# Kernel optimization log

Hardware: AMD Instinct MI355X
Metric: run time of the kernel (lower is better)

## Reference

```python
import jax, jax.numpy as jnp
import numpy as np

H_KV = 8          # num_key_value_heads (hard-coded in module)
N_HEADS = 32
HEAD_DIM = 128
GROUPS = N_HEADS // H_KV
EPS = 1e-05
ROPE_THETA = 10000.0


def rotate_half(x):
    x1, x2 = jnp.split(x, 2, axis=-1)
    return jnp.concatenate((-x2, x1), axis=-1)


def rms_norm(x, w, eps=EPS):
    xf = x.astype(jnp.float32)
    var = jnp.mean(xf * xf, axis=-1, keepdims=True)
    return (w * (xf * jax.lax.rsqrt(var + eps))).astype(x.dtype)


def setup_inputs() -> dict:
    key = jax.random.key(0)
    k1, k2, k3 = jax.random.split(key, 3)
    B, S, D = 2, 2048, 4096
    hidden_states = jax.random.normal(k1, (B, S, D), dtype=jnp.float32)
    # RoPE tables (what custom_pos_emb carries)
    inv_freq = 1.0 / (ROPE_THETA ** (jnp.arange(0, HEAD_DIM, 2, dtype=jnp.float32) / HEAD_DIM))
    t = jnp.arange(S, dtype=jnp.float32)
    freqs = jnp.outer(t, inv_freq)                 # [S, HEAD_DIM/2]
    emb = jnp.concatenate((freqs, freqs), axis=-1)  # [S, HEAD_DIM]
    cos = jnp.cos(emb)[None]                        # [1, S, HEAD_DIM]
    sin = jnp.sin(emb)[None]
    w_qkv = jax.random.normal(k2, (6144, D), dtype=jnp.float32) * 0.02
    w_o = jax.random.normal(k3, (D, D), dtype=jnp.float32) * 0.02
    q_norm_w = jnp.ones((HEAD_DIM,), dtype=jnp.float32)
    k_norm_w = jnp.ones((HEAD_DIM,), dtype=jnp.float32)
    return {"hidden_states": hidden_states, "cos": cos, "sin": sin,
            "w_qkv": w_qkv, "w_o": w_o, "q_norm_w": q_norm_w, "k_norm_w": k_norm_w}


def reference(hidden_states, cos, sin, w_qkv, w_o, q_norm_w, k_norm_w):
    B, S, D = hidden_states.shape
    qkv = hidden_states @ w_qkv.T                                    # [B,S,6144]
    qkv = qkv.reshape(B, S, H_KV, GROUPS + 2, HEAD_DIM)
    q = qkv[:, :, :, :GROUPS]                                        # [B,S,Hkv,G,d]
    k = qkv[:, :, :, GROUPS]                                         # [B,S,Hkv,d]
    v = qkv[:, :, :, GROUPS + 1]                                     # [B,S,Hkv,d]
    # to [B, heads, S, d]
    q = q.reshape(B, S, N_HEADS, HEAD_DIM).transpose(0, 2, 1, 3)     # [B,Hq,S,d]
    k = k.transpose(0, 2, 1, 3)                                      # [B,Hkv,S,d]
    v = v.transpose(0, 2, 1, 3)
    # RoPE (cos/sin: [1,S,d] -> unsqueeze head dim)
    c = cos[:, None]  # [1,1,S,d]
    s = sin[:, None]
    q = q * c + rotate_half(q) * s
    k = k * c + rotate_half(k) * s
    # per-head RMSNorm
    q = rms_norm(q, q_norm_w)
    k = rms_norm(k, k_norm_w)
    # GQA attention without materializing repeated K/V
    qg = q.reshape(B, H_KV, GROUPS, S, HEAD_DIM)
    scale = 1.0 / np.sqrt(HEAD_DIM).astype(np.float32)
    scores = jnp.einsum('bkgqd,bksd->bkgqs', qg, k) * scale          # [B,Hkv,G,S,S]
    probs = jax.nn.softmax(scores, axis=-1)
    out = jnp.einsum('bkgqs,bksd->bkgqd', probs, v)                  # [B,Hkv,G,S,d]
    out = out.reshape(B, N_HEADS, S, HEAD_DIM).transpose(0, 2, 1, 3).reshape(B, S, D)
    return out @ w_o.T
```

## Files before the change

kernel.cpp:

```cpp
#include <hip/hip_runtime.h>
#include <hip/hip_bf16.h>

typedef __attribute__((ext_vector_type(8))) short short8;
typedef __attribute__((ext_vector_type(4))) short short4v;
typedef __attribute__((ext_vector_type(4))) float floatx4;
typedef __attribute__((ext_vector_type(4))) unsigned int uintx4;

static __device__ __forceinline__ short bf16bits(float f) {
    __hip_bfloat16 h = __float2bfloat16(f);
    return __builtin_bit_cast(short, h);
}

static __device__ __forceinline__ unsigned int cvtpk(float lo, float hi) {
    unsigned int r;
    asm("v_cvt_pk_bf16_f32 %0, %1, %2" : "=v"(r) : "v"(lo), "v"(hi));
    return r;
}

#define GLDS(g, l) __builtin_amdgcn_global_load_lds( \
    (const __attribute__((address_space(1))) void*)(g), \
    (__attribute__((address_space(3))) void*)(l), 16, 0, 0)

__global__ __launch_bounds__(256) void cvt_bf16(
    const float* __restrict__ src, __hip_bfloat16* __restrict__ dst)
{
    size_t i = ((size_t)blockIdx.x * 256 + threadIdx.x) * 8;
    floatx4 f0 = *(const floatx4*)(src + i);
    floatx4 f1 = *(const floatx4*)(src + i + 4);
    short8 s;
#pragma unroll
    for (int j = 0; j < 4; j++) { s[j] = bf16bits(f0[j]); s[j + 4] = bf16bits(f1[j]); }
    *(short8*)((short*)dst + i) = s;
}

template<typename CT>
__global__ __launch_bounds__(256) void gemm_bt_fast(
    const __hip_bfloat16* __restrict__ A,
    const __hip_bfloat16* __restrict__ W,
    CT* __restrict__ C, int M, int N, int K)
{
    __shared__ alignas(16) short lA[128 * 64];
    __shared__ alignas(16) short lB[128 * 64];

    const int tid  = threadIdx.x;
    const int wave = tid >> 6;
    const int lane = tid & 63;
    const int quad = lane >> 4;
    const int l16  = lane & 15;

    const int m0 = blockIdx.x * 128;
    const int n0 = blockIdx.y * 128;
    const int wm = (wave & 1) * 64;
    const int wn = (wave >> 1) * 64;

    const int srow = lane >> 3;
    const int sblk = (lane & 7) ^ srow;
    const int scol = sblk * 8;

    const short* Ag = (const short*)A;
    const short* Wg = (const short*)W;

    floatx4 acc[4][4];
#pragma unroll
    for (int i = 0; i < 4; i++)
#pragma unroll
        for (int j = 0; j < 4; j++) acc[i][j] = (floatx4)0.0f;

    for (int k0 = 0; k0 < K; k0 += 64) {
        __syncthreads();
#pragma unroll
        for (int i = 0; i < 4; i++) {
            int c   = wave * 4 + i;
            int row = c * 8 + srow;
            GLDS(Ag + (size_t)(m0 + row) * K + k0 + scol, &lA[c * 512]);
            GLDS(Wg + (size_t)(n0 + row) * K + k0 + scol, &lB[c * 512]);
        }
        __syncthreads();
#pragma unroll
        for (int kk2 = 0; kk2 < 2; kk2++) {
            const int pb = ((kk2 * 4 + quad) ^ (l16 & 7)) * 8;
            short8 af[4], bf[4];
#pragma unroll
            for (int i = 0; i < 4; i++)
                af[i] = *(const short8*)(&lA[(wm + i * 16 + l16) * 64 + pb]);
#pragma unroll
            for (int j = 0; j < 4; j++)
                bf[j] = *(const short8*)(&lB[(wn + j * 16 + l16) * 64 + pb]);
#pragma unroll
            for (int i = 0; i < 4; i++)
#pragma unroll
                for (int j = 0; j < 4; j++)
                    acc[i][j] = __builtin_amdgcn_mfma_f32_16x16x32_bf16(
                        af[i], bf[j], acc[i][j], 0, 0, 0);
        }
    }
#pragma unroll
    for (int i = 0; i < 4; i++)
#pragma unroll
        for (int j = 0; j < 4; j++) {
            int gm = m0 + wm + i * 16 + quad * 4;
            int gn = n0 + wn + j * 16 + l16;
#pragma unroll
            for (int r = 0; r < 4; r++) {
                float v = acc[i][j][r];
                if constexpr (sizeof(CT) == 2)
                    C[(size_t)(gm + r) * N + gn] = (CT)__float2bfloat16(v);
                else
                    C[(size_t)(gm + r) * N + gn] = (CT)v;
            }
        }
}

template<bool AF32, typename CT>
__global__ __launch_bounds__(256) void gemm_bt_slow(
    const void* __restrict__ A,
    const float* __restrict__ Wf,
    CT* __restrict__ C, int M, int N, int K)
{
    __shared__ alignas(16) short lA[128 * 72];
    __shared__ alignas(16) short lB[128 * 72];

    const int tid  = threadIdx.x;
    const int wave = tid >> 6;
    const int lane = tid & 63;
    const int quad = lane >> 4;
    const int l16  = lane & 15;

    const int m0 = blockIdx.x * 128;
    const int n0 = blockIdx.y * 128;
    const int wm = (wave & 1) * 64;
    const int wn = (wave >> 1) * 64;

    floatx4 acc[4][4];
#pragma unroll
    for (int i = 0; i < 4; i++)
#pragma unroll
        for (int j = 0; j < 4; j++) acc[i][j] = (floatx4)0.0f;

    const short* Ab = (const short*)A;
    const float* Af = (const float*)A;

    for (int k0 = 0; k0 < K; k0 += 64) {
        __syncthreads();
#pragma unroll
        for (int i = 0; i < 4; i++) {
            int chunk = tid + i * 256;
            int row = chunk >> 3;
            int cc  = chunk & 7;
            if (AF32) {
                const float* src = Af + (size_t)(m0 + row) * K + k0 + cc * 8;
                floatx4 f0 = *(const floatx4*)(src);
                floatx4 f1 = *(const floatx4*)(src + 4);
                short8 s;
#pragma unroll
                for (int j = 0; j < 4; j++) { s[j] = bf16bits(f0[j]); s[j + 4] = bf16bits(f1[j]); }
                *(short8*)(&lA[row * 72 + cc * 8]) = s;
            } else {
                *(short8*)(&lA[row * 72 + cc * 8]) =
                    *(const short8*)(Ab + (size_t)(m0 + row) * K + k0 + cc * 8);
            }
            const float* src = Wf + (size_t)(n0 + row) * K + k0 + cc * 8;
            floatx4 f0 = *(const floatx4*)(src);
            floatx4 f1 = *(const floatx4*)(src + 4);
            short8 s;
#pragma unroll
            for (int j = 0; j < 4; j++) { s[j] = bf16bits(f0[j]); s[j + 4] = bf16bits(f1[j]); }
            *(short8*)(&lB[row * 72 + cc * 8]) = s;
        }
        __syncthreads();
#pragma unroll
        for (int kk = 0; kk < 64; kk += 32) {
            short8 af[4], bf[4];
#pragma unroll
            for (int i = 0; i < 4; i++)
                af[i] = *(const short8*)(&lA[(wm + i * 16 + l16) * 72 + kk + quad * 8]);
#pragma unroll
            for (int j = 0; j < 4; j++)
                bf[j] = *(const short8*)(&lB[(wn + j * 16 + l16) * 72 + kk + quad * 8]);
#pragma unroll
            for (int i = 0; i < 4; i++)
#pragma unroll
                for (int j = 0; j < 4; j++)
                    acc[i][j] = __builtin_amdgcn_mfma_f32_16x16x32_bf16(
                        af[i], bf[j], acc[i][j], 0, 0, 0);
        }
    }
#pragma unroll
    for (int i = 0; i < 4; i++)
#pragma unroll
        for (int j = 0; j < 4; j++) {
            int gm = m0 + wm + i * 16 + quad * 4;
            int gn = n0 + wn + j * 16 + l16;
#pragma unroll
            for (int r = 0; r < 4; r++) {
                float v = acc[i][j][r];
                if constexpr (sizeof(CT) == 2)
                    C[(size_t)(gm + r) * N + gn] = (CT)__float2bfloat16(v);
                else
                    C[(size_t)(gm + r) * N + gn] = (CT)v;
            }
        }
}

__global__ __launch_bounds__(256) void rope_norm(
    __hip_bfloat16* __restrict__ qkv,
    const float* __restrict__ cosb,
    const float* __restrict__ sinb,
    const float* __restrict__ qw,
    const float* __restrict__ kw)
{
    int wid  = blockIdx.x * 4 + (threadIdx.x >> 6);
    int lane = threadIdx.x & 63;
    int token = wid / 40;
    int idx   = wid % 40;
    int s = token & 2047;

    int off;
    const float* w;
    if (idx < 32) { off = (idx >> 2) * 768 + (idx & 3) * 128; w = qw; }
    else          { off = (idx - 32) * 768 + 512;             w = kw; }

    short* p = (short*)(qkv + (size_t)token * 6144 + off);
    int d = lane * 2;

    unsigned int pv = *(const unsigned int*)(p + d);
    float x0 = __builtin_bit_cast(float, pv << 16);
    float x1 = __builtin_bit_cast(float, pv & 0xffff0000u);

    float ox0 = __shfl_xor(x0, 32, 64);
    float ox1 = __shfl_xor(x1, 32, 64);

    float2 cv = *(const float2*)(cosb + s * 128 + d);
    float2 sv = *(const float2*)(sinb + s * 128 + d);
    float sgn = (lane < 32) ? -1.0f : 1.0f;
    float y0 = fmaf(sgn * ox0, sv.x, x0 * cv.x);
    float y1 = fmaf(sgn * ox1, sv.y, x1 * cv.y);

    float ss = y0 * y0 + y1 * y1;
#pragma unroll
    for (int m = 1; m < 64; m <<= 1) ss += __shfl_xor(ss, m, 64);
    float r = rsqrtf(ss * (1.0f / 128.0f) + 1e-5f);

    float2 wv = *(const float2*)(w + d);
    unsigned int out = (unsigned int)(unsigned short)bf16bits(y0 * r * wv.x)
                     | ((unsigned int)(unsigned short)bf16bits(y1 * r * wv.y) << 16);
    *(unsigned int*)(p + d) = out;
}

__global__ __launch_bounds__(256) void vtrans(
    const __hip_bfloat16* __restrict__ qkv, __hip_bfloat16* __restrict__ Vt)
{
    __shared__ alignas(16) short lT[64 * 136];

    const int bid   = blockIdx.x;
    const int stile = bid & 31;
    const int kvh   = (bid >> 5) & 7;
    const int b     = bid >> 8;
    const int tid   = threadIdx.x;
    const size_t voff = (size_t)kvh * 768 + 640;
    const short* qkvs = (const short*)qkv;

#pragma unroll
    for (int i = 0; i < 4; i++) {
        int chunk = tid + i * 256;
        int t  = chunk >> 4;
        int dc = chunk & 15;
        size_t tok = (size_t)(b * 2048 + stile * 64 + t);
        *(short8*)(&lT[t * 136 + dc * 8]) =
            *(const short8*)(qkvs + tok * 6144 + voff + dc * 8);
    }
    __syncthreads();

    int d  = tid >> 1;
    int kh = (tid & 1) * 32;
    short* out = (short*)Vt + ((size_t)((b * 8 + kvh) * 128 + d)) * 2048
               + stile * 64 + kh;
#pragma unroll
    for (int jb = 0; jb < 4; jb++) {
        short8 s;
#pragma unroll
        for (int j = 0; j < 8; j++) s[j] = lT[(kh + jb * 8 + j) * 136 + d];
        *(short8*)(out + jb * 8) = s;
    }
}

__global__ __launch_bounds__(256, 2) void attn_kernel(
    const __hip_bfloat16* __restrict__ qkv,
    const __hip_bfloat16* __restrict__ Vt,
    __hip_bfloat16* __restrict__ attn_out)
{
    __shared__ alignas(16) short lK[2][64 * 128];
    __shared__ alignas(16) short lVt[2][128 * 64];

    const int bid0 = blockIdx.x;
    const int bid  = (bid0 & 7) * 128 + (bid0 >> 3);
    const int qt   = bid & 15;
    const int h    = (bid >> 4) & 31;
    const int b    = bid >> 9;
    const int kvh  = h >> 2;
    const int lane = threadIdx.x & 63;
    const int wave = threadIdx.x >> 6;
    const int quad = lane >> 4;
    const int l16  = lane & 15;

    const size_t qoff = (size_t)kvh * 768 + (size_t)(h & 3) * 128;
    const size_t koff = (size_t)kvh * 768 + 512;
    const short* qkvs = (const short*)qkv;
    const short* Vts  = (const short*)Vt + ((size_t)(b * 8 + kvh) * 128) * 2048;

    short8 qf[2][4];
#pragma unroll
    for (int t = 0; t < 2; t++) {
        const int qrow = qt * 128 + wave * 32 + t * 16 + l16;
        const size_t qtok = (size_t)(b * 2048 + qrow);
#pragma unroll
        for (int kk = 0; kk < 4; kk++)
            qf[t][kk] = *(const short8*)(qkvs + qtok * 6144 + qoff + kk * 32 + quad * 8);
    }

    floatx4 o[2][8];
#pragma unroll
    for (int t = 0; t < 2; t++)
#pragma unroll
        for (int n = 0; n < 8; n++) o[t][n] = (floatx4)0.0f;
    float mrow[2] = { -3.0e4f, -3.0e4f };
    float lsum[2] = { 0.0f, 0.0f };

    const float scale2 = 0.08838834764831845f * 1.4426950408889634f;
    const float THR2   = 11.5418f;

    const int k_row = lane >> 4;
    const int v_row = lane >> 3;
    const int v_blk = (lane & 7) ^ v_row;

    const int srcA = l16 + ((lane & 16) << 1);
    const int srcB = srcA + 16;
    const bool hi2 = (quad >> 1) != 0;

#pragma unroll
    for (int i = 0; i < 4; i++) {
        int c = wave * 4 + i;
        int k_blk = (lane & 15) ^ ((c * 4 + k_row) & 15);
        size_t tok = (size_t)(b * 2048 + c * 4 + k_row);
        GLDS(qkvs + tok * 6144 + koff + k_blk * 8, &lK[0][c * 512]);
        int d = c * 8 + v_row;
        GLDS(Vts + (size_t)d * 2048 + v_blk * 8, &lVt[0][c * 512]);
    }

    int cur = 0;
    for (int kt = 0; kt < 32; kt++) {
        __syncthreads();

        if (kt < 31) {
            short* nK = &lK[cur ^ 1][0];
            short* nV = &lVt[cur ^ 1][0];
#pragma unroll
            for (int i = 0; i < 4; i++) {
                int c = wave * 4 + i;
                int k_blk = (lane & 15) ^ ((c * 4 + k_row) & 15);
                size_t tok = (size_t)(b * 2048 + (kt + 1) * 64 + c * 4 + k_row);
                GLDS(qkvs + tok * 6144 + koff + k_blk * 8, nK + c * 512);
                int d = c * 8 + v_row;
                GLDS(Vts + (size_t)d * 2048 + (kt + 1) * 64 + v_blk * 8, nV + c * 512);
            }
        }

        const short* lKc = &lK[cur][0];
        const short* lVc = &lVt[cur][0];

        floatx4 sc[2][4];
#pragma unroll
        for (int t = 0; t < 2; t++)
#pragma unroll
            for (int n = 0; n < 4; n++) sc[t][n] = (floatx4)0.0f;
#pragma unroll
        for (int kk = 0; kk < 4; kk++) {
#pragma unroll
            for (int n = 0; n < 4; n++) {
                short8 kf = *(const short8*)(
                    &lKc[(n * 16 + l16) * 128 + (((kk * 4 + quad) ^ l16)) * 8]);
                sc[0][n] = __builtin_amdgcn_mfma_f32_16x16x32_bf16(kf, qf[0][kk], sc[0][n], 0, 0, 0);
                sc[1][n] = __builtin_amdgcn_mfma_f32_16x16x32_bf16(kf, qf[1][kk], sc[1][n], 0, 0, 0);
            }
        }

        short8 pb[2][2];
#pragma unroll
        for (int t = 0; t < 2; t++) {
            float ma = fmaxf(fmaxf(sc[t][0][0], sc[t][0][1]), fmaxf(sc[t][0][2], sc[t][0][3]));
            float mb = fmaxf(fmaxf(sc[t][1][0], sc[t][1][1]), fmaxf(sc[t][1][2], sc[t][1][3]));
            float mc = fmaxf(fmaxf(sc[t][2][0], sc[t][2][1]), fmaxf(sc[t][2][2], sc[t][2][3]));
            float md = fmaxf(fmaxf(sc[t][3][0], sc[t][3][1]), fmaxf(sc[t][3][2], sc[t][3][3]));
            float mr = fmaxf(fmaxf(ma, mb), fmaxf(mc, md));
            mr = fmaxf(mr, __shfl_xor(mr, 16, 64));
            mr = fmaxf(mr, __shfl_xor(mr, 32, 64));
            float mx = mr * scale2;

            int grown = mx > mrow[t] + THR2;
            if (__any(grown)) {
                float mn = fmaxf(mrow[t], mx);
                float alpha = exp2f(mrow[t] - mn);
                mrow[t] = mn;
                lsum[t] *= alpha;
#pragma unroll
                for (int n = 0; n < 8; n++)
#pragma unroll
                    for (int r = 0; r < 4; r++) o[t][n][r] *= alpha;
            }

            const float nm = -mrow[t];
            float ps = 0.0f;
            unsigned int pk[4][2];
#pragma unroll
            for (int n = 0; n < 4; n++) {
#pragma unroll
                for (int r = 0; r < 4; r++) {
                    float pv = exp2f(fmaf(sc[t][n][r], scale2, nm));
                    sc[t][n][r] = pv;
                    ps += pv;
                }
                pk[n][0] = cvtpk(sc[t][n][0], sc[t][n][1]);
                pk[n][1] = cvtpk(sc[t][n][2], sc[t][n][3]);
            }
            lsum[t] += ps;

#pragma unroll
            for (int kk2 = 0; kk2 < 2; kk2++) {
                unsigned int a0 = __shfl(pk[2 * kk2][0],     srcA, 64);
                unsigned int a1 = __shfl(pk[2 * kk2 + 1][0], srcA, 64);
                unsigned int a2 = __shfl(pk[2 * kk2][1],     srcA, 64);
                unsigned int a3 = __shfl(pk[2 * kk2 + 1][1], srcA, 64);
                unsigned int c0 = __shfl(pk[2 * kk2][0],     srcB, 64);
                unsigned int c1 = __shfl(pk[2 * kk2 + 1][0], srcB, 64);
                unsigned int c2 = __shfl(pk[2 * kk2][1],     srcB, 64);
                unsigned int c3 = __shfl(pk[2 * kk2 + 1][1], srcB, 64);
                uintx4 u;
                u[0] = hi2 ? a1 : a0;
                u[1] = hi2 ? a3 : a2;
                u[2] = hi2 ? c1 : c0;
                u[3] = hi2 ? c3 : c2;
                pb[t][kk2] = __builtin_bit_cast(short8, u);
            }
        }

#pragma unroll
        for (int kk2 = 0; kk2 < 2; kk2++) {
            const int pbv = ((kk2 * 4 + quad) ^ (l16 & 7)) * 8;
#pragma unroll
            for (int n = 0; n < 8; n++) {
                short8 vf = *(const short8*)(&lVc[(n * 16 + l16) * 64 + pbv]);
                o[0][n] = __builtin_amdgcn_mfma_f32_16x16x32_bf16(vf, pb[0][kk2], o[0][n], 0, 0, 0);
                o[1][n] = __builtin_amdgcn_mfma_f32_16x16x32_bf16(vf, pb[1][kk2], o[1][n], 0, 0, 0);
            }
        }

        cur ^= 1;
    }

    float inv[2];
#pragma unroll
    for (int t = 0; t < 2; t++) {
        float s = lsum[t];
        s += __shfl_xor(s, 16, 64);
        s += __shfl_xor(s, 32, 64);
        inv[t] = 1.0f / s;
    }

#pragma unroll
    for (int t = 0; t < 2; t++) {
        const int row = qt * 128 + wave * 32 + t * 16 + l16;
        const size_t tok = (size_t)(b * 2048 + row);
        short* outp = (short*)attn_out + tok * 4096 + h * 128 + quad * 4;
#pragma unroll
        for (int n = 0; n < 8; n++) {
            short4v s4;
#pragma unroll
            for (int r = 0; r < 4; r++) s4[r] = bf16bits(o[t][n][r] * inv[t]);
            *(short4v*)(outp + n * 16) = s4;
        }
    }
}

extern "C" void kernel_launch(void* const* d_in, const int* in_sizes, int n_in,
                              void* d_out, int out_size, void* d_ws, size_t ws_size,
                              hipStream_t stream) {
    const float* hidden = (const float*)d_in[0];
    const float* cosb   = (const float*)d_in[1];
    const float* sinb   = (const float*)d_in[2];
    const float* w_qkv  = (const float*)d_in[3];
    const float* w_o    = (const float*)d_in[4];
    const float* qw     = (const float*)d_in[5];
    const float* kw     = (const float*)d_in[6];

    char* ws = (char*)d_ws;
    __hip_bfloat16* qkv    = (__hip_bfloat16*)ws;
    __hip_bfloat16* attn_o = (__hip_bfloat16*)(ws + 50331648);
    __hip_bfloat16* hb  = (__hip_bfloat16*)(ws + 83886080);
    __hip_bfloat16* wb1 = (__hip_bfloat16*)(ws + 117440512);
    __hip_bfloat16* wb2 = (__hip_bfloat16*)(ws + 167772160);
    const size_t WS_FAST = 201326592;

    __hip_bfloat16* Vt = (__hip_bfloat16*)d_out;
    float* outp        = (float*)d_out;

    const bool fast = (ws_size >= WS_FAST);

    if (fast) {
        cvt_bf16<<<16777216 / 8 / 256, 256, 0, stream>>>(hidden, hb);
        cvt_bf16<<<25165824 / 8 / 256, 256, 0, stream>>>(w_qkv, wb1);
        cvt_bf16<<<16777216 / 8 / 256, 256, 0, stream>>>(w_o, wb2);
        dim3 g1(32, 48);
        gemm_bt_fast<__hip_bfloat16><<<g1, 256, 0, stream>>>(hb, wb1, qkv, 4096, 6144, 4096);
    } else {
        dim3 g1(32, 48);
        gemm_bt_slow<true, __hip_bfloat16><<<g1, 256, 0, stream>>>(hidden, w_qkv, qkv, 4096, 6144, 4096);
    }

    rope_norm<<<40960, 256, 0, stream>>>(qkv, cosb, sinb, qw, kw);

    vtrans<<<512, 256, 0, stream>>>(qkv, Vt);

    attn_kernel<<<1024, 256, 0, stream>>>(qkv, Vt, attn_o);

    dim3 g2(32, 32);
    if (fast) {
        gemm_bt_fast<float><<<g2, 256, 0, stream>>>(attn_o, wb2, outp, 4096, 4096, 4096);
    } else {
        gemm_bt_slow<false, float><<<g2, 256, 0, stream>>>(attn_o, w_o, outp, 4096, 4096, 4096);
    }
}
```

Baseline: 875.7 us.

## Replace bf16 GEMM with 256x256 double-buffered, phase-interleaved MFMA kernel

After: 925.1 us. +5.6%, slower.

```diff
diff --git a/kernel.cpp b/kernel.cpp
--- a/kernel.cpp
+++ b/kernel.cpp
@@ -34,13 +34,13 @@
 }
 
 template<typename CT>
-__global__ __launch_bounds__(256) void gemm_bt_fast(
+__global__ __launch_bounds__(512, 2) void gemm_bt_8ph(
     const __hip_bfloat16* __restrict__ A,
     const __hip_bfloat16* __restrict__ W,
     CT* __restrict__ C, int M, int N, int K)
 {
-    __shared__ alignas(16) short lA[128 * 64];
-    __shared__ alignas(16) short lB[128 * 64];
+    __shared__ alignas(16) short lA[2][256 * 64];
+    __shared__ alignas(16) short lB[2][256 * 64];
 
     const int tid  = threadIdx.x;
     const int wave = tid >> 6;
@@ -48,10 +48,10 @@
     const int quad = lane >> 4;
     const int l16  = lane & 15;
 
-    const int m0 = blockIdx.x * 128;
-    const int n0 = blockIdx.y * 128;
-    const int wm = (wave & 1) * 64;
-    const int wn = (wave >> 1) * 64;
+    const int m0 = blockIdx.x * 256;
+    const int n0 = blockIdx.y * 256;
+    const int wm = (wave >> 2) * 128;
+    const int wn = (wave & 3) * 64;
 
     const int srow = lane >> 3;
     const int sblk = (lane & 7) ^ srow;
@@ -60,42 +60,87 @@
     const short* Ag = (const short*)A;
     const short* Wg = (const short*)W;
 
-    floatx4 acc[4][4];
-#pragma unroll
-    for (int i = 0; i < 4; i++)
+    floatx4 acc[8][4];
+#pragma unroll
+    for (int i = 0; i < 8; i++)
 #pragma unroll
         for (int j = 0; j < 4; j++) acc[i][j] = (floatx4)0.0f;
 
-    for (int k0 = 0; k0 < K; k0 += 64) {
-        __syncthreads();
-#pragma unroll
-        for (int i = 0; i < 4; i++) {
-            int c   = wave * 4 + i;
-            int row = c * 8 + srow;
-            GLDS(Ag + (size_t)(m0 + row) * K + k0 + scol, &lA[c * 512]);
-            GLDS(Wg + (size_t)(n0 + row) * K + k0 + scol, &lB[c * 512]);
-        }
-        __syncthreads();
-#pragma unroll
-        for (int kk2 = 0; kk2 < 2; kk2++) {
-            const int pb = ((kk2 * 4 + quad) ^ (l16 & 7)) * 8;
+    const int NT = K >> 6;
+
+    auto stage = [&](int t1, int p, int dst) {
+        int c   = wave * 4 + p;
+        int row = c * 8 + srow;
+        int k0  = t1 << 6;
+        GLDS(Ag + (size_t)(m0 + row) * K + k0 + scol, &lA[dst][c * 512]);
+        GLDS(Wg + (size_t)(n0 + row) * K + k0 + scol, &lB[dst][c * 512]);
+    };
+
+#pragma unroll
+    for (int p = 0; p < 4; p++) stage(0, p, 0);
+
+    int cur = 0;
+    for (int t = 0; t < NT; t++) {
+        const bool more = (t + 1 < NT);
+
+        if (more) {
+            stage(t + 1, 0, cur ^ 1);
+            asm volatile("s_waitcnt vmcnt(2)" ::: "memory");
+        } else {
+            asm volatile("s_waitcnt vmcnt(0)" ::: "memory");
+        }
+        __builtin_amdgcn_s_barrier();
+        {
+            const int pb = ((0 * 4 + quad) ^ (l16 & 7)) * 8;
             short8 af[4], bf[4];
 #pragma unroll
-            for (int i = 0; i < 4; i++)
-                af[i] = *(const short8*)(&lA[(wm + i * 16 + l16) * 64 + pb]);
+            for (int ii = 0; ii < 4; ii++)
+                af[ii] = *(const short8*)(&lA[cur][(wm + ii * 16 + l16) * 64 + pb]);
 #pragma unroll
             for (int j = 0; j < 4; j++)
-                bf[j] = *(const short8*)(&lB[(wn + j * 16 + l16) * 64 + pb]);
-#pragma unroll
-            for (int i = 0; i < 4; i++)
+                bf[j] = *(const short8*)(&lB[cur][(wn + j * 16 + l16) * 64 + pb]);
+            __builtin_amdgcn_s_setprio(1);
+#pragma unroll
+            for (int ii = 0; ii < 4; ii++)
 #pragma unroll
                 for (int j = 0; j < 4; j++)
-                    acc[i][j] = __builtin_amdgcn_mfma_f32_16x16x32_bf16(
-                        af[i], bf[j], acc[i][j], 0, 0, 0);
-        }
-    }
-#pragma unroll
-    for (int i = 0; i < 4; i++)
+                    acc[ii][j] = __builtin_amdgcn_mfma_f32_16x16x32_bf16(
+                        af[ii], bf[j], acc[ii][j], 0, 0, 0);
+            __builtin_amdgcn_s_setprio(0);
+        }
+        __builtin_amdgcn_s_barrier();
+
+#pragma unroll
+        for (int p = 1; p < 4; p++) {
+            const int kk = p >> 1;
+            const int mh = p & 1;
+            const int pb = ((kk * 4 + quad) ^ (l16 & 7)) * 8;
+            short8 af[4], bf[4];
+#pragma unroll
+            for (int ii = 0; ii < 4; ii++)
+                af[ii] = *(const short8*)(
+                    &lA[cur][(wm + (mh * 4 + ii) * 16 + l16) * 64 + pb]);
+#pragma unroll
+            for (int j = 0; j < 4; j++)
+                bf[j] = *(const short8*)(&lB[cur][(wn + j * 16 + l16) * 64 + pb]);
+            if (more) stage(t + 1, p, cur ^ 1);
+            __builtin_amdgcn_s_barrier();
+            __builtin_amdgcn_s_setprio(1);
+#pragma unroll
+            for (int ii = 0; ii < 4; ii++)
+#pragma unroll
+                for (int j = 0; j < 4; j++)
+                    acc[mh * 4 + ii][j] = __builtin_amdgcn_mfma_f32_16x16x32_bf16(
+                        af[ii], bf[j], acc[mh * 4 + ii][j], 0, 0, 0);
+            __builtin_amdgcn_s_setprio(0);
+            __builtin_amdgcn_s_barrier();
+        }
+
+        cur ^= 1;
+    }
+
+#pragma unroll
+    for (int i = 0; i < 8; i++)
 #pragma unroll
         for (int j = 0; j < 4; j++) {
             int gm = m0 + wm + i * 16 + quad * 4;
@@ -509,8 +554,8 @@
         cvt_bf16<<<16777216 / 8 / 256, 256, 0, stream>>>(hidden, hb);
         cvt_bf16<<<25165824 / 8 / 256, 256, 0, stream>>>(w_qkv, wb1);
         cvt_bf16<<<16777216 / 8 / 256, 256, 0, stream>>>(w_o, wb2);
-        dim3 g1(32, 48);
-        gemm_bt_fast<__hip_bfloat16><<<g1, 256, 0, stream>>>(hb, wb1, qkv, 4096, 6144, 4096);
+        dim3 g1(16, 24);
+        gemm_bt_8ph<__hip_bfloat16><<<g1, 512, 0, stream>>>(hb, wb1, qkv, 4096, 6144, 4096);
     } else {
         dim3 g1(32, 48);
         gemm_bt_slow<true, __hip_bfloat16><<<g1, 256, 0, stream>>>(hidden, w_qkv, qkv, 4096, 6144, 4096);
@@ -522,10 +567,11 @@
 
     attn_kernel<<<1024, 256, 0, stream>>>(qkv, Vt, attn_o);
 
-    dim3 g2(32, 32);
     if (fast) {
-        gemm_bt_fast<float><<<g2, 256, 0, stream>>>(attn_o, wb2, outp, 4096, 4096, 4096);
+        dim3 g2(16, 16);
+        gemm_bt_8ph<float><<<g2, 512, 0, stream>>>(attn_o, wb2, outp, 4096, 4096, 4096);
     } else {
+        dim3 g2(32, 32);
         gemm_bt_slow<false, float><<<g2, 256, 0, stream>>>(attn_o, w_o, outp, 4096, 4096, 4096);
     }
 }
```

## Add double-buffered 256x256-tile GEMM for output projection

Applied to the files above, without the earlier changes.

Result: faster. 837.1 us (-4.4%).

```diff
diff --git a/kernel.cpp b/kernel.cpp
--- a/kernel.cpp
+++ b/kernel.cpp
@@ -96,6 +96,98 @@
     }
 #pragma unroll
     for (int i = 0; i < 4; i++)
+#pragma unroll
+        for (int j = 0; j < 4; j++) {
+            int gm = m0 + wm + i * 16 + quad * 4;
+            int gn = n0 + wn + j * 16 + l16;
+#pragma unroll
+            for (int r = 0; r < 4; r++) {
+                float v = acc[i][j][r];
+                if constexpr (sizeof(CT) == 2)
+                    C[(size_t)(gm + r) * N + gn] = (CT)__float2bfloat16(v);
+                else
+                    C[(size_t)(gm + r) * N + gn] = (CT)v;
+            }
+        }
+}
+
+template<typename CT>
+__global__ __launch_bounds__(512, 2) void gemm_bt_dbuf(
+    const __hip_bfloat16* __restrict__ A,
+    const __hip_bfloat16* __restrict__ W,
+    CT* __restrict__ C, int M, int N, int K)
+{
+    __shared__ alignas(16) short lA[2][256 * 64];
+    __shared__ alignas(16) short lB[2][256 * 64];
+
+    const int tid  = threadIdx.x;
+    const int wave = tid >> 6;
+    const int lane = tid & 63;
+    const int quad = lane >> 4;
+    const int l16  = lane & 15;
+
+    const int m0 = blockIdx.x * 256;
+    const int n0 = blockIdx.y * 256;
+    const int wm = (wave >> 2) * 128;
+    const int wn = (wave & 3) * 64;
+
+    const int srow = lane >> 3;
+    const int sblk = (lane & 7) ^ srow;
+    const int scol = sblk * 8;
+
+    const short* Ag = (const short*)A;
+    const short* Wg = (const short*)W;
+
+    floatx4 acc[8][4];
+#pragma unroll
+    for (int i = 0; i < 8; i++)
+#pragma unroll
+        for (int j = 0; j < 4; j++) acc[i][j] = (floatx4)0.0f;
+
+    const int NT = K >> 6;
+
+    auto stage = [&](int t1, int dst) {
+        int k0 = t1 << 6;
+#pragma unroll
+        for (int p = 0; p < 4; p++) {
+            int c   = wave * 4 + p;
+            int row = c * 8 + srow;
+            GLDS(Ag + (size_t)(m0 + row) * K + k0 + scol, &lA[dst][c * 512]);
+            GLDS(Wg + (size_t)(n0 + row) * K + k0 + scol, &lB[dst][c * 512]);
+        }
+    };
+
+    stage(0, 0);
+
+    int cur = 0;
+    for (int t = 0; t < NT; t++) {
+        __syncthreads();
+        if (t + 1 < NT) stage(t + 1, cur ^ 1);
+
+#pragma unroll
+        for (int kk = 0; kk < 2; kk++) {
+            const int pb = ((kk * 4 + quad) ^ (l16 & 7)) * 8;
+            short8 bf[4], af[8];
+#pragma unroll
+            for (int j = 0; j < 4; j++)
+                bf[j] = *(const short8*)(&lB[cur][(wn + j * 16 + l16) * 64 + pb]);
+#pragma unroll
+            for (int i = 0; i < 8; i++)
+                af[i] = *(const short8*)(&lA[cur][(wm + i * 16 + l16) * 64 + pb]);
+            __builtin_amdgcn_s_setprio(1);
+#pragma unroll
+            for (int i = 0; i < 8; i++)
+#pragma unroll
+                for (int j = 0; j < 4; j++)
+                    acc[i][j] = __builtin_amdgcn_mfma_f32_16x16x32_bf16(
+                        af[i], bf[j], acc[i][j], 0, 0, 0);
+            __builtin_amdgcn_s_setprio(0);
+        }
+        cur ^= 1;
+    }
+
+#pragma unroll
+    for (int i = 0; i < 8; i++)
 #pragma unroll
         for (int j = 0; j < 4; j++) {
             int gm = m0 + wm + i * 16 + quad * 4;
@@ -522,10 +614,11 @@
 
     attn_kernel<<<1024, 256, 0, stream>>>(qkv, Vt, attn_o);
 
-    dim3 g2(32, 32);
     if (fast) {
-        gemm_bt_fast<float><<<g2, 256, 0, stream>>>(attn_o, wb2, outp, 4096, 4096, 4096);
+        dim3 g2(16, 16);
+        gemm_bt_dbuf<float><<<g2, 512, 0, stream>>>(attn_o, wb2, outp, 4096, 4096, 4096);
     } else {
+        dim3 g2(32, 32);
         gemm_bt_slow<false, float><<<g2, 256, 0, stream>>>(attn_o, w_o, outp, 4096, 4096, 4096);
     }
 }
```

## Double-buffer bf16 GEMM with larger tiles, 8 waves, and swizzled tile order

Applied to the files above, without the earlier changes.

After: 856.2 us. 2.2% less time.

```diff
diff --git a/kernel.cpp b/kernel.cpp
--- a/kernel.cpp
+++ b/kernel.cpp
@@ -33,14 +33,18 @@
     *(short8*)((short*)dst + i) = s;
 }
 
-template<typename CT>
-__global__ __launch_bounds__(256) void gemm_bt_fast(
+template<typename CT, int BM, int BN>
+__global__ __launch_bounds__(512, 2) void gemm_bt_dbuf(
     const __hip_bfloat16* __restrict__ A,
     const __hip_bfloat16* __restrict__ W,
     CT* __restrict__ C, int M, int N, int K)
 {
-    __shared__ alignas(16) short lA[128 * 64];
-    __shared__ alignas(16) short lB[128 * 64];
+    constexpr int MF = BM / 2 / 16;
+    constexpr int NF = BN / 4 / 16;
+    constexpr int CA = BM / 8;
+
+    __shared__ alignas(16) short lA[2][BM * 64];
+    __shared__ alignas(16) short lB[2][BN * 64];
 
     const int tid  = threadIdx.x;
     const int wave = tid >> 6;
@@ -48,10 +52,14 @@
     const int quad = lane >> 4;
     const int l16  = lane & 15;
 
-    const int m0 = blockIdx.x * 128;
-    const int n0 = blockIdx.y * 128;
-    const int wm = (wave & 1) * 64;
-    const int wn = (wave >> 1) * 64;
+    const int nbx  = M / BM;
+    const int q8   = gridDim.x >> 3;
+    const int tile = (blockIdx.x & 7) * q8 + (blockIdx.x >> 3);
+    const int m0 = (tile % nbx) * BM;
+    const int n0 = (tile / nbx) * BN;
+
+    const int wm = (wave >> 2) * (BM / 2);
+    const int wn = (wave & 3) * (BN / 4);
 
     const int srow = lane >> 3;
     const int sblk = (lane & 7) ^ srow;
@@ -60,44 +68,63 @@
     const short* Ag = (const short*)A;
     const short* Wg = (const short*)W;
 
-    floatx4 acc[4][4];
-#pragma unroll
-    for (int i = 0; i < 4; i++)
-#pragma unroll
-        for (int j = 0; j < 4; j++) acc[i][j] = (floatx4)0.0f;
-
-    for (int k0 = 0; k0 < K; k0 += 64) {
+    floatx4 acc[MF][NF];
+#pragma unroll
+    for (int i = 0; i < MF; i++)
+#pragma unroll
+        for (int j = 0; j < NF; j++) acc[i][j] = (floatx4)0.0f;
+
+    const int NT = K >> 6;
+
+    auto stage = [&](int t1, int dst) {
+        int k0 = t1 << 6;
+#pragma unroll
+        for (int p = 0; p < 8; p++) {
+            int c = wave * 8 + p;
+            if (c < CA) {
+                int row = c * 8 + srow;
+                GLDS(Ag + (size_t)(m0 + row) * K + k0 + scol, &lA[dst][c * 512]);
+            } else {
+                int cb  = c - CA;
+                int row = cb * 8 + srow;
+                GLDS(Wg + (size_t)(n0 + row) * K + k0 + scol, &lB[dst][cb * 512]);
+            }
+        }
+    };
+
+    stage(0, 0);
+
+    int cur = 0;
+    for (int t = 0; t < NT; t++) {
         __syncthreads();
-#pragma unroll
-        for (int i = 0; i < 4; i++) {
-            int c   = wave * 4 + i;
-            int row = c * 8 + srow;
-            GLDS(Ag + (size_t)(m0 + row) * K + k0 + scol, &lA[c * 512]);
-            GLDS(Wg + (size_t)(n0 + row) * K + k0 + scol, &lB[c * 512]);
-        }
-        __syncthreads();
-#pragma unroll
-        for (int kk2 = 0; kk2 < 2; kk2++) {
-            const int pb = ((kk2 * 4 + quad) ^ (l16 & 7)) * 8;
-            short8 af[4], bf[4];
-#pragma unroll
-            for (int i = 0; i < 4; i++)
-                af[i] = *(const short8*)(&lA[(wm + i * 16 + l16) * 64 + pb]);
-#pragma unroll
-            for (int j = 0; j < 4; j++)
-                bf[j] = *(const short8*)(&lB[(wn + j * 16 + l16) * 64 + pb]);
-#pragma unroll
-            for (int i = 0; i < 4; i++)
-#pragma unroll
-                for (int j = 0; j < 4; j++)
+        if (t + 1 < NT) stage(t + 1, cur ^ 1);
+
+#pragma unroll
+        for (int kk = 0; kk < 2; kk++) {
+            const int pb = ((kk * 4 + quad) ^ (l16 & 7)) * 8;
+            short8 bf[NF], af[MF];
+#pragma unroll
+            for (int j = 0; j < NF; j++)
+                bf[j] = *(const short8*)(&lB[cur][(wn + j * 16 + l16) * 64 + pb]);
+#pragma unroll
+            for (int i = 0; i < MF; i++)
+                af[i] = *(const short8*)(&lA[cur][(wm + i * 16 + l16) * 64 + pb]);
+            __builtin_amdgcn_s_setprio(1);
+#pragma unroll
+            for (int i = 0; i < MF; i++)
+#pragma unroll
+                for (int j = 0; j < NF; j++)
                     acc[i][j] = __builtin_amdgcn_mfma_f32_16x16x32_bf16(
                         af[i], bf[j], acc[i][j], 0, 0, 0);
-        }
-    }
-#pragma unroll
-    for (int i = 0; i < 4; i++)
-#pragma unroll
-        for (int j = 0; j < 4; j++) {
+            __builtin_amdgcn_s_setprio(0);
+        }
+        cur ^= 1;
+    }
+
+#pragma unroll
+    for (int i = 0; i < MF; i++)
+#pragma unroll
+        for (int j = 0; j < NF; j++) {
             int gm = m0 + wm + i * 16 + quad * 4;
             int gn = n0 + wn + j * 16 + l16;
 #pragma unroll
@@ -509,8 +536,8 @@
         cvt_bf16<<<16777216 / 8 / 256, 256, 0, stream>>>(hidden, hb);
         cvt_bf16<<<25165824 / 8 / 256, 256, 0, stream>>>(w_qkv, wb1);
         cvt_bf16<<<16777216 / 8 / 256, 256, 0, stream>>>(w_o, wb2);
-        dim3 g1(32, 48);
-        gemm_bt_fast<__hip_bfloat16><<<g1, 256, 0, stream>>>(hb, wb1, qkv, 4096, 6144, 4096);
+        gemm_bt_dbuf<__hip_bfloat16, 128, 384><<<512, 512, 0, stream>>>(
+            hb, wb1, qkv, 4096, 6144, 4096);
     } else {
         dim3 g1(32, 48);
         gemm_bt_slow<true, __hip_bfloat16><<<g1, 256, 0, stream>>>(hidden, w_qkv, qkv, 4096, 6144, 4096);
@@ -522,10 +549,11 @@
 
     attn_kernel<<<1024, 256, 0, stream>>>(qkv, Vt, attn_o);
 
-    dim3 g2(32, 32);
     if (fast) {
-        gemm_bt_fast<float><<<g2, 256, 0, stream>>>(attn_o, wb2, outp, 4096, 4096, 4096);
+        gemm_bt_dbuf<float, 256, 256><<<256, 512, 0, stream>>>(
+            attn_o, wb2, outp, 4096, 4096, 4096);
     } else {
+        dim3 g2(32, 32);
         gemm_bt_slow<false, float><<<g2, 256, 0, stream>>>(attn_o, w_o, outp, 4096, 4096, 4096);
     }
 }
```
